# Optimization experiments

Hardware: AMD Instinct MI355X
Metric: run time of the kernel (lower is better)

Reference implementation:

```python
import jax, jax.numpy as jnp
import numpy as np

N_RNA, N_ATAC = 4096, 8192
IN_C, HID, H = 256, 128, 2
DH = HID // H
TOPK, THR = 10, 0.8


def setup_inputs() -> dict:
    key = jax.random.key(0)
    ks = jax.random.split(key, 16)
    s = 0.02
    inp = {
        'x_rna': jax.random.normal(ks[0], (N_RNA, IN_C), jnp.float32),
        'x_atac': jax.random.normal(ks[1], (N_ATAC, IN_C), jnp.float32),
        'chrom_mask': (jax.random.uniform(ks[2], (N_RNA, N_ATAC)) > 0.5).astype(jnp.float32),
        'Wq': jax.random.normal(ks[3], (IN_C, HID)) * s, 'bq': jnp.zeros((HID,)),
        'Wk': jax.random.normal(ks[4], (IN_C, HID)) * s, 'bk': jnp.zeros((HID,)),
        'Wvr': jax.random.normal(ks[5], (IN_C, HID)) * s, 'bvr': jnp.zeros((HID,)),
        'Wva': jax.random.normal(ks[6], (IN_C, HID)) * s, 'bva': jnp.zeros((HID,)),
        'Wor': jax.random.normal(ks[7], (HID, HID)) * s, 'bor': jnp.zeros((HID,)),
        'Woa': jax.random.normal(ks[8], (HID, HID)) * s, 'boa': jnp.zeros((HID,)),
        'Wsr': jax.random.normal(ks[9], (IN_C, HID)) * s, 'bsr': jnp.zeros((HID,)),
        'Wsa': jax.random.normal(ks[10], (IN_C, HID)) * s, 'bsa': jnp.zeros((HID,)),
        'Wdr': jax.random.normal(ks[11], (2 * HID, HID)) * s, 'bdr': jnp.zeros((HID,)),
        'Wda': jax.random.normal(ks[12], (2 * HID, HID)) * s, 'bda': jnp.zeros((HID,)),
    }
    return inp


def reference(x_rna, x_atac, chrom_mask, Wq, bq, Wk, bk, Wvr, bvr, Wva, bva,
              Wor, bor, Woa, boa, Wsr, bsr, Wsa, bsa, Wdr, bdr, Wda, bda):
    # projections -> [N, H, DH]
    q = (x_rna @ Wq + bq).reshape(N_RNA, H, DH)
    k = (x_atac @ Wk + bk).reshape(N_ATAC, H, DH)
    v_a = (x_atac @ Wva + bva).reshape(N_ATAC, H, DH)
    v_r = (x_rna @ Wvr + bvr).reshape(N_RNA, H, DH)

    # raw attention [H, N_rna, N_atac], biological mask, sigmoid
    att = jnp.einsum('rhd,ahd->hra', q, k) * chrom_mask[None]
    att = jax.nn.sigmoid(att)
    thr_mask = (att > THR).astype(att.dtype)

    # top-k sparsify + softmax over selected values, scatter back
    topv, topi = jax.lax.top_k(att, TOPK)          # [H, N_rna, K]
    topv = jax.nn.softmax(topv, axis=-1)
    i_h = jnp.arange(H)[:, None, None]
    i_r = jnp.arange(N_RNA)[None, :, None]
    sparse = jnp.zeros_like(att).at[i_h, i_r, topi].set(topv)
    att = sparse * thr_mask

    # aggregations (second bmm and its transpose)
    rna_agg = jnp.einsum('hra,ahd->rhd', att, v_a).reshape(N_RNA, HID)
    atac_agg = jnp.einsum('hra,rhd->ahd', att, v_r).reshape(N_ATAC, HID)

    # out proj (num_heads > 1), self attention concat, dim reduction
    rna_agg = rna_agg @ Wor + bor
    atac_agg = atac_agg @ Woa + boa
    rna_agg = jnp.concatenate([rna_agg, x_rna @ Wsr + bsr], axis=1)
    atac_agg = jnp.concatenate([atac_agg, x_atac @ Wsa + bsa], axis=1)
    return (rna_agg @ Wdr + bdr, atac_agg @ Wda + bda)
```

## Files before the change

kernel.cpp:

```cpp
#include <hip/hip_runtime.h>
#include <math.h>

#define N_RNA 4096
#define N_ATAC 8192
#define IN_C 256
#define HID 128
#define NH 2
#define TOPK 10
#define CAP 32
#define NCHUNK 8
#define TAU_EPS 0.12f
#define NEG_INF -3.402823466e38f

typedef __attribute__((ext_vector_type(8))) short bf16x8;
typedef __attribute__((ext_vector_type(4))) float f32x4;

static __device__ __forceinline__ f32x4 mfma16(bf16x8 a, bf16x8 b, f32x4 c) {
    return __builtin_amdgcn_mfma_f32_16x16x32_bf16(a, b, c, 0, 0, 0);
}

static __device__ __forceinline__ unsigned short f2bf(float f) {
    unsigned int u = __float_as_uint(f);
    unsigned int r = (u + 0x7fffu + ((u >> 16) & 1u)) >> 16;
    return (unsigned short)r;
}
static __device__ __forceinline__ float bf2f(unsigned short h) {
    return __uint_as_float(((unsigned int)h) << 16);
}

__global__ __launch_bounds__(256) void prep_all(
    const float* __restrict__ mask, unsigned int* __restrict__ bits2,
    float* __restrict__ atac_agg,
    const float* __restrict__ Wor, const float* __restrict__ bor,
    const float* __restrict__ Woa, const float* __restrict__ boa,
    const float* __restrict__ Wsr, const float* __restrict__ bsr,
    const float* __restrict__ Wsa, const float* __restrict__ bsa,
    const float* __restrict__ Wdr, const float* __restrict__ bdr,
    const float* __restrict__ Wda, const float* __restrict__ bda,
    float* __restrict__ Wr1, float* __restrict__ Wr2, float* __restrict__ br,
    float* __restrict__ Wa1, float* __restrict__ Wa2, float* __restrict__ ba,
    const float* __restrict__ x_rna, const float* __restrict__ x_atac,
    const float* __restrict__ Wq, const float* __restrict__ bq,
    const float* __restrict__ Wk, const float* __restrict__ bk,
    const float* __restrict__ Wvr, const float* __restrict__ bvr,
    const float* __restrict__ Wva, const float* __restrict__ bva,
    unsigned short* __restrict__ qhi, unsigned short* __restrict__ qlo,
    unsigned short* __restrict__ khf_hi, unsigned short* __restrict__ khf_lo,
    float* __restrict__ v_r, float* __restrict__ v_a) {
    __shared__ __align__(16) float x_s[32][33];
    __shared__ __align__(16) float w_s[32][128];
    int bx = blockIdx.x;
    int tid = threadIdx.x;

    if (bx >= 768 && bx < 1792) {
        int e = bx - 768;
        int rt = e >> 4, ac = e & 15;
        int a0 = ac * 512 + tid * 2;
        int r0 = rt * 64;
        unsigned int w0[2] = {0, 0}, w1[2] = {0, 0};
#pragma unroll 8
        for (int rr = 0; rr < 32; ++rr) {
            float2 m0 = *(const float2*)&mask[(size_t)(r0 + rr) * N_ATAC + a0];
            float2 m1 = *(const float2*)&mask[(size_t)(r0 + 32 + rr) * N_ATAC + a0];
            w0[0] |= ((m0.x > 0.5f) ? 1u : 0u) << rr;
            w0[1] |= ((m0.y > 0.5f) ? 1u : 0u) << rr;
            w1[0] |= ((m1.x > 0.5f) ? 1u : 0u) << rr;
            w1[1] |= ((m1.y > 0.5f) ? 1u : 0u) << rr;
        }
        uint4 o = make_uint4(w0[0], w1[0], w0[1], w1[1]);
        *(uint4*)&bits2[((size_t)rt * N_ATAC + a0) * 2] = o;
        return;
    }
    if (bx >= 1792 && bx < 2048) {
        size_t i = ((size_t)(bx - 1792) * 256 + tid) * 16;
        float4 z = make_float4(0.f, 0.f, 0.f, 0.f);
        *(float4*)&atac_agg[i] = z;
        *(float4*)&atac_agg[i + 4] = z;
        *(float4*)&atac_agg[i + 8] = z;
        *(float4*)&atac_agg[i + 12] = z;
        return;
    }
    if (bx >= 2048) {
        int f = (bx - 2048) * 256 + tid;
        if (f < 16384) {
            int i = f >> 7, j = f & 127; float s = 0.f;
            for (int t = 0; t < 128; ++t) s += Wor[i * 128 + t] * Wdr[t * 128 + j];
            Wr1[f] = s;
        } else if (f < 49152) {
            int e = f - 16384; int i = e >> 7, j = e & 127; float s = 0.f;
            for (int t = 0; t < 128; ++t) s += Wsr[i * 128 + t] * Wdr[(128 + t) * 128 + j];
            Wr2[e] = s;
        } else if (f < 65536) {
            int e = f - 49152; int i = e >> 7, j = e & 127; float s = 0.f;
            for (int t = 0; t < 128; ++t) s += Woa[i * 128 + t] * Wda[t * 128 + j];
            Wa1[e] = s;
        } else if (f < 98304) {
            int e = f - 65536; int i = e >> 7, j = e & 127; float s = 0.f;
            for (int t = 0; t < 128; ++t) s += Wsa[i * 128 + t] * Wda[(128 + t) * 128 + j];
            Wa2[e] = s;
        } else if (f < 98432) {
            int j = f - 98304; float s = bdr[j];
            for (int t = 0; t < 128; ++t) s += bor[t] * Wdr[t * 128 + j] + bsr[t] * Wdr[(128 + t) * 128 + j];
            br[j] = s;
        } else if (f < 98560) {
            int j = f - 98432; float s = bda[j];
            for (int t = 0; t < 128; ++t) s += boa[t] * Wda[t * 128 + j] + bsa[t] * Wda[(128 + t) * 128 + j];
            ba[j] = s;
        }
        return;
    }

    int e = bx;
    int cfg, rblk;
    if (e < 128)      { cfg = 0; rblk = e; }
    else if (e < 256) { cfg = 1; rblk = e - 128; }
    else if (e < 512) { cfg = 2; rblk = e - 256; }
    else              { cfg = 3; rblk = e - 512; }
    const float *X, *W, *B;
    if (cfg == 0)      { X = x_rna;  W = Wq;  B = bq;  }
    else if (cfg == 1) { X = x_rna;  W = Wvr; B = bvr; }
    else if (cfg == 2) { X = x_atac; W = Wk;  B = bk;  }
    else               { X = x_atac; W = Wva; B = bva; }
    int r0 = rblk * 32;
    int rg = tid >> 4, cg = tid & 15;

    float acc[2][8];
#pragma unroll
    for (int i = 0; i < 2; ++i)
#pragma unroll
        for (int j = 0; j < 8; ++j) acc[i][j] = 0.f;

    for (int k0 = 0; k0 < IN_C; k0 += 32) {
        __syncthreads();
        {
            int rr = tid >> 3, kq = tid & 7;
            float4 v = *(const float4*)&X[(size_t)(r0 + rr) * IN_C + k0 + kq * 4];
            x_s[rr][kq * 4 + 0] = v.x; x_s[rr][kq * 4 + 1] = v.y;
            x_s[rr][kq * 4 + 2] = v.z; x_s[rr][kq * 4 + 3] = v.w;
        }
        for (int i4 = tid; i4 < 1024; i4 += 256) {
            int kk = i4 >> 5, cq = i4 & 31;
            float4 v = *(const float4*)&W[(size_t)(k0 + kk) * HID + cq * 4];
            *(float4*)&w_s[kk][cq * 4] = v;
        }
        __syncthreads();
#pragma unroll 8
        for (int kk = 0; kk < 32; ++kk) {
            float x0 = x_s[rg * 2 + 0][kk], x1 = x_s[rg * 2 + 1][kk];
            float4 wa = *(const float4*)&w_s[kk][cg * 4];
            float4 wb = *(const float4*)&w_s[kk][64 + cg * 4];
            acc[0][0] += x0 * wa.x; acc[0][1] += x0 * wa.y; acc[0][2] += x0 * wa.z; acc[0][3] += x0 * wa.w;
            acc[0][4] += x0 * wb.x; acc[0][5] += x0 * wb.y; acc[0][6] += x0 * wb.z; acc[0][7] += x0 * wb.w;
            acc[1][0] += x1 * wa.x; acc[1][1] += x1 * wa.y; acc[1][2] += x1 * wa.z; acc[1][3] += x1 * wa.w;
            acc[1][4] += x1 * wb.x; acc[1][5] += x1 * wb.y; acc[1][6] += x1 * wb.z; acc[1][7] += x1 * wb.w;
        }
    }
    float bv[8];
#pragma unroll
    for (int j = 0; j < 8; ++j) {
        int c = (j < 4) ? (cg * 4 + j) : (64 + cg * 4 + (j - 4));
        bv[j] = B[c];
    }
    if (cfg == 0 || cfg == 2) {
#pragma unroll
        for (int i = 0; i < 2; ++i) {
            int r = r0 + rg * 2 + i;
            float va[8];
#pragma unroll
            for (int j = 0; j < 8; ++j) va[j] = acc[i][j] + bv[j];
            ushort4 h0, l0, h1, l1;
            h0.x = f2bf(va[0]); h0.y = f2bf(va[1]); h0.z = f2bf(va[2]); h0.w = f2bf(va[3]);
            h1.x = f2bf(va[4]); h1.y = f2bf(va[5]); h1.z = f2bf(va[6]); h1.w = f2bf(va[7]);
            l0.x = f2bf(va[0] - bf2f(h0.x)); l0.y = f2bf(va[1] - bf2f(h0.y));
            l0.z = f2bf(va[2] - bf2f(h0.z)); l0.w = f2bf(va[3] - bf2f(h0.w));
            l1.x = f2bf(va[4] - bf2f(h1.x)); l1.y = f2bf(va[5] - bf2f(h1.y));
            l1.z = f2bf(va[6] - bf2f(h1.z)); l1.w = f2bf(va[7] - bf2f(h1.w));
            if (cfg == 0) {
                size_t o0 = (size_t)r * 64 + cg * 4;
                size_t o1 = (size_t)(N_RNA + r) * 64 + cg * 4;
                *(ushort4*)&qhi[o0] = h0; *(ushort4*)&qhi[o1] = h1;
                *(ushort4*)&qlo[o0] = l0; *(ushort4*)&qlo[o1] = l1;
            } else {
                int at = r >> 4, n = r & 15;
                int kc = cg >> 1, ee = (cg & 1) * 4;
                size_t o0 = ((size_t)(at) * 8 + kc) * 128 + n * 8 + ee;
                size_t o1 = ((size_t)(512 + at) * 8 + kc) * 128 + n * 8 + ee;
                *(ushort4*)&khf_hi[o0] = h0; *(ushort4*)&khf_hi[o1] = h1;
                *(ushort4*)&khf_lo[o0] = l0; *(ushort4*)&khf_lo[o1] = l1;
            }
        }
    } else {
        float* C = (cfg == 1) ? v_r : v_a;
#pragma unroll
        for (int i = 0; i < 2; ++i) {
            int r = r0 + rg * 2 + i;
            float4 oa = make_float4(acc[i][0] + bv[0], acc[i][1] + bv[1], acc[i][2] + bv[2], acc[i][3] + bv[3]);
            float4 ob = make_float4(acc[i][4] + bv[4], acc[i][5] + bv[5], acc[i][6] + bv[6], acc[i][7] + bv[7]);
            *(float4*)&C[(size_t)r * HID + cg * 4] = oa;
            *(float4*)&C[(size_t)r * HID + 64 + cg * 4] = ob;
        }
    }
}

__global__ __launch_bounds__(256, 4) void attn2(
    const unsigned short* __restrict__ qhi, const unsigned short* __restrict__ qlo,
    const unsigned short* __restrict__ khf_hi, const unsigned short* __restrict__ khf_lo,
    const unsigned int* __restrict__ bits2,
    int* __restrict__ scnt, float* __restrict__ sval, int* __restrict__ sidx) {
    int hq = blockIdx.x; int h = hq >> 3, chunk = hq & 7;
    int rt = blockIdx.y; int r0 = rt * 32;
    int tid = threadIdx.x;
    int w = tid >> 6, lane = tid & 63;
    int n = lane & 15, quad = lane >> 4;
    int q4 = quad * 4;
    int at0 = chunk * 64 + w * 16;
    int hbase = h * 512;
    int rt64 = rt >> 1, word = rt & 1;

    __shared__ __align__(16) float smem[32 * 65];
    __shared__ float taus[32];
    __shared__ int   lcnt[32];

    const bf16x8* kh8 = (const bf16x8*)khf_hi;
    const bf16x8* kl8 = (const bf16x8*)khf_lo;

    bf16x8 Ah[2][2], Al[2][2];
#pragma unroll
    for (int mt = 0; mt < 2; ++mt)
#pragma unroll
        for (int c = 0; c < 2; ++c) {
            size_t off = ((size_t)h * N_RNA + r0 + mt * 16 + n) * 64 + c * 32 + quad * 8;
            Ah[mt][c] = *(const bf16x8*)(qhi + off);
            Al[mt][c] = *(const bf16x8*)(qlo + off);
        }

    float mx[2][4];
#pragma unroll
    for (int mt = 0; mt < 2; ++mt)
#pragma unroll
        for (int i = 0; i < 4; ++i) mx[mt][i] = 0.f;

#pragma unroll 2
    for (int t = 0; t < 16; ++t) {
        int at = at0 + t;
        size_t bidx = ((size_t)hbase + at) * 128 + lane;
        bf16x8 Bh0 = kh8[bidx];
        bf16x8 Bh1 = kh8[bidx + 64];
        unsigned int bw = bits2[((size_t)rt64 * N_ATAC + at * 16 + n) * 2 + word];

        f32x4 S[2];
#pragma unroll
        for (int mt = 0; mt < 2; ++mt) {
            f32x4 s = {0.f, 0.f, 0.f, 0.f};
            s = mfma16(Ah[mt][0], Bh0, s);
            s = mfma16(Ah[mt][1], Bh1, s);
            S[mt] = s;
        }
#pragma unroll
        for (int mt = 0; mt < 2; ++mt) {
            unsigned int sh = bw >> ((mt << 4) + q4);
#pragma unroll
            for (int i = 0; i < 4; ++i) {
                float v = ((sh >> i) & 1) ? S[mt][i] : 0.f;
                mx[mt][i] = fmaxf(mx[mt][i], v);
            }
        }
    }

    {
        int b = w * 16 + n;
#pragma unroll
        for (int mt = 0; mt < 2; ++mt)
#pragma unroll
            for (int i = 0; i < 4; ++i) smem[(mt * 16 + q4 + i) * 65 + b] = mx[mt][i];
    }
    __syncthreads();
    {
        int row = tid >> 3, sub = tid & 7;
        float v[8];
#pragma unroll
        for (int j = 0; j < 8; ++j) v[j] = smem[row * 65 + sub * 8 + j];
        float t10 = 0.f;
#pragma unroll
        for (int s = 0; s < 10; ++s) {
            float bv = v[0]; int bj = 0;
#pragma unroll
            for (int j = 1; j < 8; ++j) if (v[j] > bv) { bv = v[j]; bj = j; }
            int meta = (sub << 3) | bj;
#pragma unroll
            for (int off = 1; off < 8; off <<= 1) {
                float ov = __shfl_xor(bv, off);
                int om = __shfl_xor(meta, off);
                if (ov > bv || (ov == bv && om < meta)) { bv = ov; meta = om; }
            }
            if ((meta >> 3) == sub) v[meta & 7] = -1.f;
            t10 = bv;
        }
        if (sub == 0) taus[row] = t10 - TAU_EPS;
        if (tid < 32) lcnt[tid] = 0;
    }
    __syncthreads();

    float tau[2][4];
#pragma unroll
    for (int mt = 0; mt < 2; ++mt)
#pragma unroll
        for (int i = 0; i < 4; ++i) tau[mt][i] = taus[mt * 16 + q4 + i];

    float* lval = smem;
    int*   lidx = (int*)(smem + 1024);

#pragma unroll 2
    for (int t = 0; t < 16; ++t) {
        int at = at0 + t;
        size_t bidx = ((size_t)hbase + at) * 128 + lane;
        bf16x8 Bh0 = kh8[bidx];
        bf16x8 Bh1 = kh8[bidx + 64];
        bf16x8 Bl0 = kl8[bidx];
        bf16x8 Bl1 = kl8[bidx + 64];
        unsigned int bw = bits2[((size_t)rt64 * N_ATAC + at * 16 + n) * 2 + word];

        f32x4 S[2];
#pragma unroll
        for (int mt = 0; mt < 2; ++mt) {
            f32x4 s = {0.f, 0.f, 0.f, 0.f};
            s = mfma16(Ah[mt][0], Bh0, s);
            s = mfma16(Ah[mt][1], Bh1, s);
            s = mfma16(Ah[mt][0], Bl0, s);
            s = mfma16(Ah[mt][1], Bl1, s);
            s = mfma16(Al[mt][0], Bh0, s);
            s = mfma16(Al[mt][1], Bh1, s);
            S[mt] = s;
        }
        int a16 = at * 16 + n;
#pragma unroll
        for (int mt = 0; mt < 2; ++mt) {
            unsigned int sh = bw >> ((mt << 4) + q4);
#pragma unroll
            for (int i = 0; i < 4; ++i) {
                if (((sh >> i) & 1) && S[mt][i] >= tau[mt][i]) {
                    int row = mt * 16 + q4 + i;
                    int pos = atomicAdd(&lcnt[row], 1);
                    if (pos < CAP) { lval[row * CAP + pos] = S[mt][i]; lidx[row * CAP + pos] = a16; }
                }
            }
        }
    }
    __syncthreads();

    if (tid < 32) {
        int c = lcnt[tid]; if (c > CAP) c = CAP;
        scnt[((size_t)h * N_RNA + r0 + tid) * NCHUNK + chunk] = c;
    }
    {
        int row = tid >> 3, j0 = tid & 7;
        int c = lcnt[row]; if (c > CAP) c = CAP;
        size_t slot = ((size_t)h * N_RNA + r0 + row) * NCHUNK + chunk;
        for (int j = j0; j < c; j += 8) {
            sval[slot * CAP + j] = lval[row * CAP + j];
            sidx[slot * CAP + j] = lidx[row * CAP + j];
        }
    }
}

__global__ __launch_bounds__(256) void fin_agg(
    const int* __restrict__ scnt, const float* __restrict__ sval, const int* __restrict__ sidx,
    const float* __restrict__ v_a, const float* __restrict__ v_r,
    float* __restrict__ rna_agg, float* __restrict__ atac_agg) {
    int wid = threadIdx.x >> 6, lane = threadIdx.x & 63;
    int p = blockIdx.x * 4 + wid;
    int h = p >> 12, r = p & 4095;
    size_t sbase = (size_t)p * NCHUNK;

    float val[4]; int aidx[4];
#pragma unroll
    for (int j = 0; j < 4; ++j) {
        int e = j * 64 + lane;
        int chunk = e >> 5, pos = e & 31;
        int c = scnt[sbase + chunk];
        size_t sl = (sbase + chunk) * CAP + pos;
        bool ok = pos < c;
        val[j] = ok ? sval[sl] : NEG_INF;
        aidx[j] = ok ? sidx[sl] : 0;
    }

    float sv[10]; int si[10];
#pragma unroll
    for (int s = 0; s < 10; ++s) {
        float bv = val[0]; int bj = 0;
#pragma unroll
        for (int j = 1; j < 4; ++j) if (val[j] > bv) { bv = val[j]; bj = j; }
        int bmeta = (bj << 6) | lane;
#pragma unroll
        for (int off = 32; off >= 1; off >>= 1) {
            float ov = __shfl_xor(bv, off);
            int om = __shfl_xor(bmeta, off);
            if (ov > bv || (ov == bv && om < bmeta)) { bv = ov; bmeta = om; }
        }
        int wj = bmeta >> 6, wl = bmeta & 63;
        if (lane == wl) {
#pragma unroll
            for (int j = 0; j < 4; ++j) if (j == wj) val[j] = NEG_INF;
        }
        int av = aidx[0];
#pragma unroll
        for (int j = 1; j < 4; ++j) if (wj == j) av = aidx[j];
        sv[s] = bv;
        si[s] = __shfl(av, wl);
    }

    float wgt[10]; float sum = 0.f; float sg[10];
#pragma unroll
    for (int s = 0; s < 10; ++s) {
        sg[s] = 1.0f / (1.0f + expf(-sv[s]));
        float es = expf(sg[s]);
        wgt[s] = es;
        sum += es;
    }
    float inv = 1.0f / sum;
#pragma unroll
    for (int s = 0; s < 10; ++s) {
        wgt[s] *= inv;
        if (!(sg[s] > 0.8f)) wgt[s] = 0.f;
    }

    float acc = 0.f;
#pragma unroll
    for (int s = 0; s < 10; ++s) {
        float vv = v_a[(size_t)si[s] * HID + h * 64 + lane];
        acc += wgt[s] * vv;
    }
    rna_agg[(size_t)r * HID + h * 64 + lane] = acc;

    float vr = v_r[(size_t)r * HID + h * 64 + lane];
#pragma unroll
    for (int s = 0; s < 10; ++s) {
        if (wgt[s] != 0.f) {
            atomicAdd(&atac_agg[(size_t)si[s] * HID + h * 64 + lane], wgt[s] * vr);
        }
    }
}

__global__ __launch_bounds__(256) void out_gemm(
    const float* __restrict__ rna_agg, const float* __restrict__ x_rna,
    const float* __restrict__ Wr1, const float* __restrict__ Wr2, const float* __restrict__ brf,
    const float* __restrict__ atac_agg, const float* __restrict__ x_atac,
    const float* __restrict__ Wa1, const float* __restrict__ Wa2, const float* __restrict__ baf,
    float* __restrict__ out_r, float* __restrict__ out_a) {
    __shared__ __align__(16) float x_s[32][33];
    __shared__ __align__(16) float w_s[32][128];
    int bx = blockIdx.x;
    const float *A, *X, *W1, *W2, *bias; float* C;
    int r0;
    if (bx < 128) { A = rna_agg; X = x_rna; W1 = Wr1; W2 = Wr2; bias = brf; C = out_r; r0 = bx * 32; }
    else { A = atac_agg; X = x_atac; W1 = Wa1; W2 = Wa2; bias = baf; C = out_a; r0 = (bx - 128) * 32; }
    int tid = threadIdx.x;
    int rg = tid >> 4, cg = tid & 15;

    float acc[2][8];
#pragma unroll
    for (int i = 0; i < 2; ++i)
#pragma unroll
        for (int j = 0; j < 8; ++j) acc[i][j] = 0.f;

    for (int k0 = 0; k0 < 384; k0 += 32) {
        __syncthreads();
        {
            int rr = tid >> 3, kq = tid & 7;
            float4 v;
            if (k0 < 128) v = *(const float4*)&A[(size_t)(r0 + rr) * HID + k0 + kq * 4];
            else          v = *(const float4*)&X[(size_t)(r0 + rr) * IN_C + (k0 - 128) + kq * 4];
            x_s[rr][kq * 4 + 0] = v.x; x_s[rr][kq * 4 + 1] = v.y;
            x_s[rr][kq * 4 + 2] = v.z; x_s[rr][kq * 4 + 3] = v.w;
        }
        for (int i4 = tid; i4 < 1024; i4 += 256) {
            int kk = i4 >> 5, cq = i4 & 31;
            float4 v;
            if (k0 < 128) v = *(const float4*)&W1[(size_t)(k0 + kk) * HID + cq * 4];
            else          v = *(const float4*)&W2[(size_t)(k0 - 128 + kk) * HID + cq * 4];
            *(float4*)&w_s[kk][cq * 4] = v;
        }
        __syncthreads();
#pragma unroll 8
        for (int kk = 0; kk < 32; ++kk) {
            float x0 = x_s[rg * 2 + 0][kk], x1 = x_s[rg * 2 + 1][kk];
            float4 wa = *(const float4*)&w_s[kk][cg * 4];
            float4 wb = *(const float4*)&w_s[kk][64 + cg * 4];
            acc[0][0] += x0 * wa.x; acc[0][1] += x0 * wa.y; acc[0][2] += x0 * wa.z; acc[0][3] += x0 * wa.w;
            acc[0][4] += x0 * wb.x; acc[0][5] += x0 * wb.y; acc[0][6] += x0 * wb.z; acc[0][7] += x0 * wb.w;
            acc[1][0] += x1 * wa.x; acc[1][1] += x1 * wa.y; acc[1][2] += x1 * wa.z; acc[1][3] += x1 * wa.w;
            acc[1][4] += x1 * wb.x; acc[1][5] += x1 * wb.y; acc[1][6] += x1 * wb.z; acc[1][7] += x1 * wb.w;
        }
    }
    float bv[8];
#pragma unroll
    for (int j = 0; j < 8; ++j) {
        int c = (j < 4) ? (cg * 4 + j) : (64 + cg * 4 + (j - 4));
        bv[j] = bias[c];
    }
#pragma unroll
    for (int i = 0; i < 2; ++i) {
        int r = r0 + rg * 2 + i;
        float4 oa = make_float4(acc[i][0] + bv[0], acc[i][1] + bv[1], acc[i][2] + bv[2], acc[i][3] + bv[3]);
        float4 ob = make_float4(acc[i][4] + bv[4], acc[i][5] + bv[5], acc[i][6] + bv[6], acc[i][7] + bv[7]);
        *(float4*)&C[(size_t)r * HID + cg * 4] = oa;
        *(float4*)&C[(size_t)r * HID + 64 + cg * 4] = ob;
    }
}

extern "C" void kernel_launch(void* const* d_in, const int* in_sizes, int n_in,
                              void* d_out, int out_size, void* d_ws, size_t ws_size,
                              hipStream_t stream) {
    const float* x_rna = (const float*)d_in[0];
    const float* x_atac = (const float*)d_in[1];
    const float* mask = (const float*)d_in[2];
    const float* Wq = (const float*)d_in[3];  const float* bq = (const float*)d_in[4];
    const float* Wk = (const float*)d_in[5];  const float* bk = (const float*)d_in[6];
    const float* Wvr = (const float*)d_in[7]; const float* bvr = (const float*)d_in[8];
    const float* Wva = (const float*)d_in[9]; const float* bva = (const float*)d_in[10];
    const float* Wor = (const float*)d_in[11]; const float* bor = (const float*)d_in[12];
    const float* Woa = (const float*)d_in[13]; const float* boa = (const float*)d_in[14];
    const float* Wsr = (const float*)d_in[15]; const float* bsr = (const float*)d_in[16];
    const float* Wsa = (const float*)d_in[17]; const float* bsa = (const float*)d_in[18];
    const float* Wdr = (const float*)d_in[19]; const float* bdr = (const float*)d_in[20];
    const float* Wda = (const float*)d_in[21]; const float* bda = (const float*)d_in[22];

    float* out_r = (float*)d_out;
    float* out_a = out_r + N_RNA * HID;

    float* ws = (float*)d_ws;
    unsigned short* qhi = (unsigned short*)ws;
    unsigned short* qlo = qhi + 524288;
    unsigned short* khf_hi = qlo + 524288;
    unsigned short* khf_lo = khf_hi + 1048576;
    unsigned int* bits2 = (unsigned int*)(ws + 1572864);
    float* v_r = ws + 1572864 + 1048576;
    float* v_a = v_r + 524288;
    float* Wr1 = v_a + 1048576;
    float* Wr2 = Wr1 + 16384;
    float* brf = Wr2 + 32768;
    float* Wa1 = brf + 128;
    float* Wa2 = Wa1 + 16384;
    float* baf = Wa2 + 32768;
    int* scnt = (int*)(baf + 128);
    float* sval = (float*)scnt + 65536;
    int* sidx = (int*)(sval + 2097152);
    float* rna_agg = (float*)sidx + 2097152;
    float* atac_agg = rna_agg + 524288;

    hipLaunchKernelGGL(prep_all, dim3(2434), dim3(256), 0, stream,
                       mask, bits2, atac_agg,
                       Wor, bor, Woa, boa, Wsr, bsr, Wsa, bsa, Wdr, bdr, Wda, bda,
                       Wr1, Wr2, brf, Wa1, Wa2, baf,
                       x_rna, x_atac, Wq, bq, Wk, bk, Wvr, bvr, Wva, bva,
                       qhi, qlo, khf_hi, khf_lo, v_r, v_a);
    hipLaunchKernelGGL(attn2, dim3(16, 128), dim3(256), 0, stream,
                       qhi, qlo, khf_hi, khf_lo, bits2, scnt, sval, sidx);
    hipLaunchKernelGGL(fin_agg, dim3(2048), dim3(256), 0, stream,
                       scnt, sval, sidx, v_a, v_r, rna_agg, atac_agg);
    hipLaunchKernelGGL(out_gemm, dim3(384), dim3(256), 0, stream,
                       rna_agg, x_rna, Wr1, Wr2, brf,
                       atac_agg, x_atac, Wa1, Wa2, baf, out_r, out_a);
}
```

Baseline: 420.4 us.

## Move projection and output GEMMs to split-bf16 MFMA with pre-transposed weights

Replaces the FP32 FMA inner loops of the input projections and the fused output GEMM with bf16 MFMA, using a hi/lo split (three MFMAs per tile) to keep near-FP32 accuracy. A new wprep kernel transposes and splits the weights into bf16 hi/lo arrays ahead of time and folds the weight-combining products. The mask bit-packing blocks also now process four columns per thread. This adds an extra kernel launch and scalar scattered epilogue stores in exchange for much cheaper matrix math.

```diff
diff --git a/kernel.cpp b/kernel.cpp
--- a/kernel.cpp
+++ b/kernel.cpp
@@ -28,51 +28,129 @@
     return __uint_as_float(((unsigned int)h) << 16);
 }
 
-__global__ __launch_bounds__(256) void prep_all(
-    const float* __restrict__ mask, unsigned int* __restrict__ bits2,
-    float* __restrict__ atac_agg,
+__global__ __launch_bounds__(256) void wprep(
+    const float* __restrict__ Wq, const float* __restrict__ Wk,
+    const float* __restrict__ Wvr, const float* __restrict__ Wva,
     const float* __restrict__ Wor, const float* __restrict__ bor,
     const float* __restrict__ Woa, const float* __restrict__ boa,
     const float* __restrict__ Wsr, const float* __restrict__ bsr,
     const float* __restrict__ Wsa, const float* __restrict__ bsa,
     const float* __restrict__ Wdr, const float* __restrict__ bdr,
     const float* __restrict__ Wda, const float* __restrict__ bda,
-    float* __restrict__ Wr1, float* __restrict__ Wr2, float* __restrict__ br,
-    float* __restrict__ Wa1, float* __restrict__ Wa2, float* __restrict__ ba,
+    unsigned short* __restrict__ wt, unsigned short* __restrict__ wrf,
+    unsigned short* __restrict__ waf,
+    float* __restrict__ brf, float* __restrict__ baf) {
+    int bx = blockIdx.x, tid = threadIdx.x;
+    if (bx < 32) {
+        int cfg = bx >> 3, k0 = (bx & 7) * 32;
+        const float* W = (cfg == 0) ? Wq : (cfg == 1) ? Wvr : (cfg == 2) ? Wk : Wva;
+        __shared__ float ts[32][132];
+#pragma unroll
+        for (int rep = 0; rep < 4; ++rep) {
+            int id = rep * 256 + tid; int kk = id >> 5, cq = id & 31;
+            float4 v = *(const float4*)&W[(size_t)(k0 + kk) * HID + cq * 4];
+            ts[kk][cq * 4 + 0] = v.x; ts[kk][cq * 4 + 1] = v.y;
+            ts[kk][cq * 4 + 2] = v.z; ts[kk][cq * 4 + 3] = v.w;
+        }
+        __syncthreads();
+        int col = tid >> 1, seg = tid & 1;
+        unsigned short hb[16], lb[16];
+#pragma unroll
+        for (int u = 0; u < 16; ++u) {
+            float f = ts[seg * 16 + u][col];
+            unsigned short h = f2bf(f);
+            hb[u] = h; lb[u] = f2bf(f - bf2f(h));
+        }
+        unsigned short* hp = wt + cfg * 65536;
+        unsigned short* lp = hp + 32768;
+        size_t o = (size_t)col * 256 + k0 + seg * 16;
+#pragma unroll
+        for (int u4 = 0; u4 < 4; ++u4) {
+            ushort4 th, tl;
+            th.x = hb[u4 * 4]; th.y = hb[u4 * 4 + 1]; th.z = hb[u4 * 4 + 2]; th.w = hb[u4 * 4 + 3];
+            tl.x = lb[u4 * 4]; tl.y = lb[u4 * 4 + 1]; tl.z = lb[u4 * 4 + 2]; tl.w = lb[u4 * 4 + 3];
+            *(ushort4*)&hp[o + u4 * 4] = th;
+            *(ushort4*)&lp[o + u4 * 4] = tl;
+        }
+        return;
+    }
+    int f = (bx - 32) * 256 + tid;
+    if (f < 16384) {
+        int i = f >> 7, j = f & 127; float s = 0.f;
+        for (int t = 0; t < 128; ++t) s += Wor[i * 128 + t] * Wdr[t * 128 + j];
+        unsigned short h = f2bf(s);
+        wrf[(size_t)j * 128 + i] = h;
+        wrf[16384 + (size_t)j * 128 + i] = f2bf(s - bf2f(h));
+    } else if (f < 49152) {
+        int e = f - 16384; int i = e >> 7, j = e & 127; float s = 0.f;
+        for (int t = 0; t < 128; ++t) s += Wsr[i * 128 + t] * Wdr[(128 + t) * 128 + j];
+        unsigned short h = f2bf(s);
+        wrf[32768 + (size_t)j * 256 + i] = h;
+        wrf[65536 + (size_t)j * 256 + i] = f2bf(s - bf2f(h));
+    } else if (f < 65536) {
+        int e = f - 49152; int i = e >> 7, j = e & 127; float s = 0.f;
+        for (int t = 0; t < 128; ++t) s += Woa[i * 128 + t] * Wda[t * 128 + j];
+        unsigned short h = f2bf(s);
+        waf[(size_t)j * 128 + i] = h;
+        waf[16384 + (size_t)j * 128 + i] = f2bf(s - bf2f(h));
+    } else if (f < 98304) {
+        int e = f - 65536; int i = e >> 7, j = e & 127; float s = 0.f;
+        for (int t = 0; t < 128; ++t) s += Wsa[i * 128 + t] * Wda[(128 + t) * 128 + j];
+        unsigned short h = f2bf(s);
+        waf[32768 + (size_t)j * 256 + i] = h;
+        waf[65536 + (size_t)j * 256 + i] = f2bf(s - bf2f(h));
+    } else if (f < 98432) {
+        int j = f - 98304; float s = bdr[j];
+        for (int t = 0; t < 128; ++t) s += bor[t] * Wdr[t * 128 + j] + bsr[t] * Wdr[(128 + t) * 128 + j];
+        brf[j] = s;
+    } else if (f < 98560) {
+        int j = f - 98432; float s = bda[j];
+        for (int t = 0; t < 128; ++t) s += boa[t] * Wda[t * 128 + j] + bsa[t] * Wda[(128 + t) * 128 + j];
+        baf[j] = s;
+    }
+}
+
+__global__ __launch_bounds__(256) void prep_all(
+    const float* __restrict__ mask, unsigned int* __restrict__ bits2,
+    float* __restrict__ atac_agg,
     const float* __restrict__ x_rna, const float* __restrict__ x_atac,
-    const float* __restrict__ Wq, const float* __restrict__ bq,
-    const float* __restrict__ Wk, const float* __restrict__ bk,
-    const float* __restrict__ Wvr, const float* __restrict__ bvr,
-    const float* __restrict__ Wva, const float* __restrict__ bva,
+    const unsigned short* __restrict__ wt,
+    const float* __restrict__ bq, const float* __restrict__ bk,
+    const float* __restrict__ bvr, const float* __restrict__ bva,
     unsigned short* __restrict__ qhi, unsigned short* __restrict__ qlo,
     unsigned short* __restrict__ khf_hi, unsigned short* __restrict__ khf_lo,
     float* __restrict__ v_r, float* __restrict__ v_a) {
-    __shared__ __align__(16) float x_s[32][33];
-    __shared__ __align__(16) float w_s[32][128];
-    int bx = blockIdx.x;
-    int tid = threadIdx.x;
-
-    if (bx >= 768 && bx < 1792) {
+    __shared__ __align__(16) unsigned short ah_s[32 * 40];
+    __shared__ __align__(16) unsigned short al_s[32 * 40];
+    int bx = blockIdx.x, tid = threadIdx.x;
+
+    if (bx >= 768 && bx < 1280) {
         int e = bx - 768;
-        int rt = e >> 4, ac = e & 15;
-        int a0 = ac * 512 + tid * 2;
+        int rt = e >> 3, ac = e & 7;
+        int a0 = ac * 1024 + tid * 4;
         int r0 = rt * 64;
-        unsigned int w0[2] = {0, 0}, w1[2] = {0, 0};
+        unsigned int w0[4] = {0, 0, 0, 0}, w1[4] = {0, 0, 0, 0};
 #pragma unroll 8
         for (int rr = 0; rr < 32; ++rr) {
-            float2 m0 = *(const float2*)&mask[(size_t)(r0 + rr) * N_ATAC + a0];
-            float2 m1 = *(const float2*)&mask[(size_t)(r0 + 32 + rr) * N_ATAC + a0];
+            float4 m0 = *(const float4*)&mask[(size_t)(r0 + rr) * N_ATAC + a0];
+            float4 m1 = *(const float4*)&mask[(size_t)(r0 + 32 + rr) * N_ATAC + a0];
             w0[0] |= ((m0.x > 0.5f) ? 1u : 0u) << rr;
             w0[1] |= ((m0.y > 0.5f) ? 1u : 0u) << rr;
+            w0[2] |= ((m0.z > 0.5f) ? 1u : 0u) << rr;
+            w0[3] |= ((m0.w > 0.5f) ? 1u : 0u) << rr;
             w1[0] |= ((m1.x > 0.5f) ? 1u : 0u) << rr;
             w1[1] |= ((m1.y > 0.5f) ? 1u : 0u) << rr;
-        }
-        uint4 o = make_uint4(w0[0], w1[0], w0[1], w1[1]);
-        *(uint4*)&bits2[((size_t)rt * N_ATAC + a0) * 2] = o;
+            w1[2] |= ((m1.z > 0.5f) ? 1u : 0u) << rr;
+            w1[3] |= ((m1.w > 0.5f) ? 1u : 0u) << rr;
+        }
+        uint4 oA = make_uint4(w0[0], w1[0], w0[1], w1[1]);
+        uint4 oB = make_uint4(w0[2], w1[2], w0[3], w1[3]);
+        *(uint4*)&bits2[((size_t)rt * N_ATAC + a0) * 2] = oA;
+        *(uint4*)&bits2[((size_t)rt * N_ATAC + a0) * 2 + 4] = oB;
         return;
     }
-    if (bx >= 1792 && bx < 2048) {
-        size_t i = ((size_t)(bx - 1792) * 256 + tid) * 16;
+    if (bx >= 1280) {
+        size_t i = ((size_t)(bx - 1280) * 256 + tid) * 16;
         float4 z = make_float4(0.f, 0.f, 0.f, 0.f);
         *(float4*)&atac_agg[i] = z;
         *(float4*)&atac_agg[i + 4] = z;
@@ -80,125 +158,104 @@
         *(float4*)&atac_agg[i + 12] = z;
         return;
     }
-    if (bx >= 2048) {
-        int f = (bx - 2048) * 256 + tid;
-        if (f < 16384) {
-            int i = f >> 7, j = f & 127; float s = 0.f;
-            for (int t = 0; t < 128; ++t) s += Wor[i * 128 + t] * Wdr[t * 128 + j];
-            Wr1[f] = s;
-        } else if (f < 49152) {
-            int e = f - 16384; int i = e >> 7, j = e & 127; float s = 0.f;
-            for (int t = 0; t < 128; ++t) s += Wsr[i * 128 + t] * Wdr[(128 + t) * 128 + j];
-            Wr2[e] = s;
-        } else if (f < 65536) {
-            int e = f - 49152; int i = e >> 7, j = e & 127; float s = 0.f;
-            for (int t = 0; t < 128; ++t) s += Woa[i * 128 + t] * Wda[t * 128 + j];
-            Wa1[e] = s;
-        } else if (f < 98304) {
-            int e = f - 65536; int i = e >> 7, j = e & 127; float s = 0.f;
-            for (int t = 0; t < 128; ++t) s += Wsa[i * 128 + t] * Wda[(128 + t) * 128 + j];
-            Wa2[e] = s;
-        } else if (f < 98432) {
-            int j = f - 98304; float s = bdr[j];
-            for (int t = 0; t < 128; ++t) s += bor[t] * Wdr[t * 128 + j] + bsr[t] * Wdr[(128 + t) * 128 + j];
-            br[j] = s;
-        } else if (f < 98560) {
-            int j = f - 98432; float s = bda[j];
-            for (int t = 0; t < 128; ++t) s += boa[t] * Wda[t * 128 + j] + bsa[t] * Wda[(128 + t) * 128 + j];
-            ba[j] = s;
-        }
-        return;
-    }
-
-    int e = bx;
+
     int cfg, rblk;
-    if (e < 128)      { cfg = 0; rblk = e; }
-    else if (e < 256) { cfg = 1; rblk = e - 128; }
-    else if (e < 512) { cfg = 2; rblk = e - 256; }
-    else              { cfg = 3; rblk = e - 512; }
-    const float *X, *W, *B;
-    if (cfg == 0)      { X = x_rna;  W = Wq;  B = bq;  }
-    else if (cfg == 1) { X = x_rna;  W = Wvr; B = bvr; }
-    else if (cfg == 2) { X = x_atac; W = Wk;  B = bk;  }
-    else               { X = x_atac; W = Wva; B = bva; }
+    if (bx < 128)      { cfg = 0; rblk = bx; }
+    else if (bx < 256) { cfg = 1; rblk = bx - 128; }
+    else if (bx < 512) { cfg = 2; rblk = bx - 256; }
+    else               { cfg = 3; rblk = bx - 512; }
+    const float* X = (cfg <= 1) ? x_rna : x_atac;
+    const float* Bv = (cfg == 0) ? bq : (cfg == 1) ? bvr : (cfg == 2) ? bk : bva;
+    const unsigned short* wth = wt + cfg * 65536;
+    const unsigned short* wtl = wth + 32768;
     int r0 = rblk * 32;
-    int rg = tid >> 4, cg = tid & 15;
-
-    float acc[2][8];
-#pragma unroll
-    for (int i = 0; i < 2; ++i)
-#pragma unroll
-        for (int j = 0; j < 8; ++j) acc[i][j] = 0.f;
+    int w = tid >> 6, lane = tid & 63, n = lane & 15, quad = lane >> 4;
+
+    const f32x4 zf = {0.f, 0.f, 0.f, 0.f};
+    f32x4 acc[2][2];
+#pragma unroll
+    for (int mt = 0; mt < 2; ++mt)
+#pragma unroll
+        for (int nt = 0; nt < 2; ++nt) acc[mt][nt] = zf;
 
     for (int k0 = 0; k0 < IN_C; k0 += 32) {
         __syncthreads();
         {
             int rr = tid >> 3, kq = tid & 7;
             float4 v = *(const float4*)&X[(size_t)(r0 + rr) * IN_C + k0 + kq * 4];
-            x_s[rr][kq * 4 + 0] = v.x; x_s[rr][kq * 4 + 1] = v.y;
-            x_s[rr][kq * 4 + 2] = v.z; x_s[rr][kq * 4 + 3] = v.w;
-        }
-        for (int i4 = tid; i4 < 1024; i4 += 256) {
-            int kk = i4 >> 5, cq = i4 & 31;
-            float4 v = *(const float4*)&W[(size_t)(k0 + kk) * HID + cq * 4];
-            *(float4*)&w_s[kk][cq * 4] = v;
+            ushort4 h, l;
+            h.x = f2bf(v.x); h.y = f2bf(v.y); h.z = f2bf(v.z); h.w = f2bf(v.w);
+            l.x = f2bf(v.x - bf2f(h.x)); l.y = f2bf(v.y - bf2f(h.y));
+            l.z = f2bf(v.z - bf2f(h.z)); l.w = f2bf(v.w - bf2f(h.w));
+            *(ushort4*)&ah_s[rr * 40 + kq * 4] = h;
+            *(ushort4*)&al_s[rr * 40 + kq * 4] = l;
         }
         __syncthreads();
-#pragma unroll 8
-        for (int kk = 0; kk < 32; ++kk) {
-            float x0 = x_s[rg * 2 + 0][kk], x1 = x_s[rg * 2 + 1][kk];
-            float4 wa = *(const float4*)&w_s[kk][cg * 4];
-            float4 wb = *(const float4*)&w_s[kk][64 + cg * 4];
-            acc[0][0] += x0 * wa.x; acc[0][1] += x0 * wa.y; acc[0][2] += x0 * wa.z; acc[0][3] += x0 * wa.w;
-            acc[0][4] += x0 * wb.x; acc[0][5] += x0 * wb.y; acc[0][6] += x0 * wb.z; acc[0][7] += x0 * wb.w;
-            acc[1][0] += x1 * wa.x; acc[1][1] += x1 * wa.y; acc[1][2] += x1 * wa.z; acc[1][3] += x1 * wa.w;
-            acc[1][4] += x1 * wb.x; acc[1][5] += x1 * wb.y; acc[1][6] += x1 * wb.z; acc[1][7] += x1 * wb.w;
-        }
-    }
-    float bv[8];
-#pragma unroll
-    for (int j = 0; j < 8; ++j) {
-        int c = (j < 4) ? (cg * 4 + j) : (64 + cg * 4 + (j - 4));
-        bv[j] = B[c];
-    }
-    if (cfg == 0 || cfg == 2) {
-#pragma unroll
-        for (int i = 0; i < 2; ++i) {
-            int r = r0 + rg * 2 + i;
-            float va[8];
-#pragma unroll
-            for (int j = 0; j < 8; ++j) va[j] = acc[i][j] + bv[j];
-            ushort4 h0, l0, h1, l1;
-            h0.x = f2bf(va[0]); h0.y = f2bf(va[1]); h0.z = f2bf(va[2]); h0.w = f2bf(va[3]);
-            h1.x = f2bf(va[4]); h1.y = f2bf(va[5]); h1.z = f2bf(va[6]); h1.w = f2bf(va[7]);
-            l0.x = f2bf(va[0] - bf2f(h0.x)); l0.y = f2bf(va[1] - bf2f(h0.y));
-            l0.z = f2bf(va[2] - bf2f(h0.z)); l0.w = f2bf(va[3] - bf2f(h0.w));
-            l1.x = f2bf(va[4] - bf2f(h1.x)); l1.y = f2bf(va[5] - bf2f(h1.y));
-            l1.z = f2bf(va[6] - bf2f(h1.z)); l1.w = f2bf(va[7] - bf2f(h1.w));
-            if (cfg == 0) {
-                size_t o0 = (size_t)r * 64 + cg * 4;
-                size_t o1 = (size_t)(N_RNA + r) * 64 + cg * 4;
-                *(ushort4*)&qhi[o0] = h0; *(ushort4*)&qhi[o1] = h1;
-                *(ushort4*)&qlo[o0] = l0; *(ushort4*)&qlo[o1] = l1;
-            } else {
-                int at = r >> 4, n = r & 15;
-                int kc = cg >> 1, ee = (cg & 1) * 4;
-                size_t o0 = ((size_t)(at) * 8 + kc) * 128 + n * 8 + ee;
-                size_t o1 = ((size_t)(512 + at) * 8 + kc) * 128 + n * 8 + ee;
-                *(ushort4*)&khf_hi[o0] = h0; *(ushort4*)&khf_hi[o1] = h1;
-                *(ushort4*)&khf_lo[o0] = l0; *(ushort4*)&khf_lo[o1] = l1;
+        bf16x8 Afh[2], Afl[2];
+#pragma unroll
+        for (int mt = 0; mt < 2; ++mt) {
+            Afh[mt] = *(const bf16x8*)&ah_s[(mt * 16 + n) * 40 + quad * 8];
+            Afl[mt] = *(const bf16x8*)&al_s[(mt * 16 + n) * 40 + quad * 8];
+        }
+#pragma unroll
+        for (int nt = 0; nt < 2; ++nt) {
+            int c = w * 32 + nt * 16 + n;
+            size_t o = (size_t)c * 256 + k0 + quad * 8;
+            bf16x8 Bh = *(const bf16x8*)&wth[o];
+            bf16x8 Bl = *(const bf16x8*)&wtl[o];
+#pragma unroll
+            for (int mt = 0; mt < 2; ++mt) {
+                acc[mt][nt] = mfma16(Afh[mt], Bh, acc[mt][nt]);
+                acc[mt][nt] = mfma16(Afh[mt], Bl, acc[mt][nt]);
+                acc[mt][nt] = mfma16(Afl[mt], Bh, acc[mt][nt]);
             }
         }
+    }
+    float bvx[2];
+    bvx[0] = Bv[w * 32 + n]; bvx[1] = Bv[w * 32 + 16 + n];
+    if (cfg == 1 || cfg == 3) {
+        float* C = (cfg == 1) ? v_r : v_a;
+#pragma unroll
+        for (int mt = 0; mt < 2; ++mt)
+#pragma unroll
+            for (int nt = 0; nt < 2; ++nt)
+#pragma unroll
+                for (int i = 0; i < 4; ++i) {
+                    int r = r0 + mt * 16 + quad * 4 + i;
+                    int c = w * 32 + nt * 16 + n;
+                    C[(size_t)r * HID + c] = acc[mt][nt][i] + bvx[nt];
+                }
+    } else if (cfg == 0) {
+#pragma unroll
+        for (int mt = 0; mt < 2; ++mt)
+#pragma unroll
+            for (int nt = 0; nt < 2; ++nt)
+#pragma unroll
+                for (int i = 0; i < 4; ++i) {
+                    int r = r0 + mt * 16 + quad * 4 + i;
+                    int c = w * 32 + nt * 16 + n;
+                    float o = acc[mt][nt][i] + bvx[nt];
+                    int head = c >> 6, ch = c & 63;
+                    size_t off = ((size_t)head * N_RNA + r) * 64 + ch;
+                    unsigned short h = f2bf(o);
+                    qhi[off] = h; qlo[off] = f2bf(o - bf2f(h));
+                }
     } else {
-        float* C = (cfg == 1) ? v_r : v_a;
-#pragma unroll
-        for (int i = 0; i < 2; ++i) {
-            int r = r0 + rg * 2 + i;
-            float4 oa = make_float4(acc[i][0] + bv[0], acc[i][1] + bv[1], acc[i][2] + bv[2], acc[i][3] + bv[3]);
-            float4 ob = make_float4(acc[i][4] + bv[4], acc[i][5] + bv[5], acc[i][6] + bv[6], acc[i][7] + bv[7]);
-            *(float4*)&C[(size_t)r * HID + cg * 4] = oa;
-            *(float4*)&C[(size_t)r * HID + 64 + cg * 4] = ob;
-        }
+#pragma unroll
+        for (int mt = 0; mt < 2; ++mt)
+#pragma unroll
+            for (int nt = 0; nt < 2; ++nt)
+#pragma unroll
+                for (int i = 0; i < 4; ++i) {
+                    int r = r0 + mt * 16 + quad * 4 + i;
+                    int c = w * 32 + nt * 16 + n;
+                    float o = acc[mt][nt][i] + bvx[nt];
+                    int head = c >> 6, ch = c & 63;
+                    size_t off = ((size_t)(head * 512 + (r >> 4)) * 8 + (ch >> 3)) * 128
+                               + (size_t)(r & 15) * 8 + (ch & 7);
+                    unsigned short h = f2bf(o);
+                    khf_hi[off] = h; khf_lo[off] = f2bf(o - bf2f(h));
+                }
     }
 }
 
@@ -443,25 +500,24 @@
 
 __global__ __launch_bounds__(256) void out_gemm(
     const float* __restrict__ rna_agg, const float* __restrict__ x_rna,
-    const float* __restrict__ Wr1, const float* __restrict__ Wr2, const float* __restrict__ brf,
+    const unsigned short* __restrict__ wrt, const float* __restrict__ brf,
     const float* __restrict__ atac_agg, const float* __restrict__ x_atac,
-    const float* __restrict__ Wa1, const float* __restrict__ Wa2, const float* __restrict__ baf,
+    const unsigned short* __restrict__ wat, const float* __restrict__ baf,
     float* __restrict__ out_r, float* __restrict__ out_a) {
-    __shared__ __align__(16) float x_s[32][33];
-    __shared__ __align__(16) float w_s[32][128];
-    int bx = blockIdx.x;
-    const float *A, *X, *W1, *W2, *bias; float* C;
-    int r0;
-    if (bx < 128) { A = rna_agg; X = x_rna; W1 = Wr1; W2 = Wr2; bias = brf; C = out_r; r0 = bx * 32; }
-    else { A = atac_agg; X = x_atac; W1 = Wa1; W2 = Wa2; bias = baf; C = out_a; r0 = (bx - 128) * 32; }
-    int tid = threadIdx.x;
-    int rg = tid >> 4, cg = tid & 15;
-
-    float acc[2][8];
-#pragma unroll
-    for (int i = 0; i < 2; ++i)
-#pragma unroll
-        for (int j = 0; j < 8; ++j) acc[i][j] = 0.f;
+    __shared__ __align__(16) unsigned short ah_s[32 * 40];
+    __shared__ __align__(16) unsigned short al_s[32 * 40];
+    int bx = blockIdx.x, tid = threadIdx.x;
+    const float *A, *X, *bias; const unsigned short* wb; float* C; int r0;
+    if (bx < 128) { A = rna_agg; X = x_rna; wb = wrt; bias = brf; C = out_r; r0 = bx * 32; }
+    else { A = atac_agg; X = x_atac; wb = wat; bias = baf; C = out_a; r0 = (bx - 128) * 32; }
+    int w = tid >> 6, lane = tid & 63, n = lane & 15, quad = lane >> 4;
+
+    const f32x4 zf = {0.f, 0.f, 0.f, 0.f};
+    f32x4 acc[2][2];
+#pragma unroll
+    for (int mt = 0; mt < 2; ++mt)
+#pragma unroll
+        for (int nt = 0; nt < 2; ++nt) acc[mt][nt] = zf;
 
     for (int k0 = 0; k0 < 384; k0 += 32) {
         __syncthreads();
@@ -470,42 +526,49 @@
             float4 v;
             if (k0 < 128) v = *(const float4*)&A[(size_t)(r0 + rr) * HID + k0 + kq * 4];
             else          v = *(const float4*)&X[(size_t)(r0 + rr) * IN_C + (k0 - 128) + kq * 4];
-            x_s[rr][kq * 4 + 0] = v.x; x_s[rr][kq * 4 + 1] = v.y;
-            x_s[rr][kq * 4 + 2] = v.z; x_s[rr][kq * 4 + 3] = v.w;
-        }
-        for (int i4 = tid; i4 < 1024; i4 += 256) {
-            int kk = i4 >> 5, cq = i4 & 31;
-            float4 v;
-            if (k0 < 128) v = *(const float4*)&W1[(size_t)(k0 + kk) * HID + cq * 4];
-            else          v = *(const float4*)&W2[(size_t)(k0 - 128 + kk) * HID + cq * 4];
-            *(float4*)&w_s[kk][cq * 4] = v;
+            ushort4 h, l;
+            h.x = f2bf(v.x); h.y = f2bf(v.y); h.z = f2bf(v.z); h.w = f2bf(v.w);
+            l.x = f2bf(v.x - bf2f(h.x)); l.y = f2bf(v.y - bf2f(h.y));
+            l.z = f2bf(v.z - bf2f(h.z)); l.w = f2bf(v.w - bf2f(h.w));
+            *(ushort4*)&ah_s[rr * 40 + kq * 4] = h;
+            *(ushort4*)&al_s[rr * 40 + kq * 4] = l;
         }
         __syncthreads();
-#pragma unroll 8
-        for (int kk = 0; kk < 32; ++kk) {
-            float x0 = x_s[rg * 2 + 0][kk], x1 = x_s[rg * 2 + 1][kk];
-            float4 wa = *(const float4*)&w_s[kk][cg * 4];
-            float4 wb = *(const float4*)&w_s[kk][64 + cg * 4];
-            acc[0][0] += x0 * wa.x; acc[0][1] += x0 * wa.y; acc[0][2] += x0 * wa.z; acc[0][3] += x0 * wa.w;
-            acc[0][4] += x0 * wb.x; acc[0][5] += x0 * wb.y; acc[0][6] += x0 * wb.z; acc[0][7] += x0 * wb.w;
-            acc[1][0] += x1 * wa.x; acc[1][1] += x1 * wa.y; acc[1][2] += x1 * wa.z; acc[1][3] += x1 * wa.w;
-            acc[1][4] += x1 * wb.x; acc[1][5] += x1 * wb.y; acc[1][6] += x1 * wb.z; acc[1][7] += x1 * wb.w;
-        }
-    }
-    float bv[8];
-#pragma unroll
-    for (int j = 0; j < 8; ++j) {
-        int c = (j < 4) ? (cg * 4 + j) : (64 + cg * 4 + (j - 4));
-        bv[j] = bias[c];
-    }
-#pragma unroll
-    for (int i = 0; i < 2; ++i) {
-        int r = r0 + rg * 2 + i;
-        float4 oa = make_float4(acc[i][0] + bv[0], acc[i][1] + bv[1], acc[i][2] + bv[2], acc[i][3] + bv[3]);
-        float4 ob = make_float4(acc[i][4] + bv[4], acc[i][5] + bv[5], acc[i][6] + bv[6], acc[i][7] + bv[7]);
-        *(float4*)&C[(size_t)r * HID + cg * 4] = oa;
-        *(float4*)&C[(size_t)r * HID + 64 + cg * 4] = ob;
-    }
+        bf16x8 Afh[2], Afl[2];
+#pragma unroll
+        for (int mt = 0; mt < 2; ++mt) {
+            Afh[mt] = *(const bf16x8*)&ah_s[(mt * 16 + n) * 40 + quad * 8];
+            Afl[mt] = *(const bf16x8*)&al_s[(mt * 16 + n) * 40 + quad * 8];
+        }
+#pragma unroll
+        for (int nt = 0; nt < 2; ++nt) {
+            int c = w * 32 + nt * 16 + n;
+            size_t o;
+            const unsigned short *ph, *pl;
+            if (k0 < 128) { o = (size_t)c * 128 + k0 + quad * 8;         ph = wb;         pl = wb + 16384; }
+            else          { o = (size_t)c * 256 + (k0 - 128) + quad * 8; ph = wb + 32768; pl = wb + 65536; }
+            bf16x8 Bh = *(const bf16x8*)&ph[o];
+            bf16x8 Bl = *(const bf16x8*)&pl[o];
+#pragma unroll
+            for (int mt = 0; mt < 2; ++mt) {
+                acc[mt][nt] = mfma16(Afh[mt], Bh, acc[mt][nt]);
+                acc[mt][nt] = mfma16(Afh[mt], Bl, acc[mt][nt]);
+                acc[mt][nt] = mfma16(Afl[mt], Bh, acc[mt][nt]);
+            }
+        }
+    }
+    float bvx[2];
+    bvx[0] = bias[w * 32 + n]; bvx[1] = bias[w * 32 + 16 + n];
+#pragma unroll
+    for (int mt = 0; mt < 2; ++mt)
+#pragma unroll
+        for (int nt = 0; nt < 2; ++nt)
+#pragma unroll
+            for (int i = 0; i < 4; ++i) {
+                int r = r0 + mt * 16 + quad * 4 + i;
+                int c = w * 32 + nt * 16 + n;
+                C[(size_t)r * HID + c] = acc[mt][nt][i] + bvx[nt];
+            }
 }
 
 extern "C" void kernel_launch(void* const* d_in, const int* in_sizes, int n_in,
@@ -547,18 +610,24 @@
     int* sidx = (int*)(sval + 2097152);
     float* rna_agg = (float*)sidx + 2097152;
     float* atac_agg = rna_agg + 524288;
-
-    hipLaunchKernelGGL(prep_all, dim3(2434), dim3(256), 0, stream,
-                       mask, bits2, atac_agg,
+    unsigned short* wt = (unsigned short*)(atac_agg + 1048576);
+
+    unsigned short* wrf = (unsigned short*)Wr1;
+    unsigned short* waf = (unsigned short*)Wa1;
+
+    hipLaunchKernelGGL(wprep, dim3(417), dim3(256), 0, stream,
+                       Wq, Wk, Wvr, Wva,
                        Wor, bor, Woa, boa, Wsr, bsr, Wsa, bsa, Wdr, bdr, Wda, bda,
-                       Wr1, Wr2, brf, Wa1, Wa2, baf,
-                       x_rna, x_atac, Wq, bq, Wk, bk, Wvr, bvr, Wva, bva,
+                       wt, wrf, waf, brf, baf);
+    hipLaunchKernelGGL(prep_all, dim3(1536), dim3(256), 0, stream,
+                       mask, bits2, atac_agg, x_rna, x_atac, wt,
+                       bq, bk, bvr, bva,
                        qhi, qlo, khf_hi, khf_lo, v_r, v_a);
     hipLaunchKernelGGL(attn2, dim3(16, 128), dim3(256), 0, stream,
                        qhi, qlo, khf_hi, khf_lo, bits2, scnt, sval, sidx);
     hipLaunchKernelGGL(fin_agg, dim3(2048), dim3(256), 0, stream,
                        scnt, sval, sidx, v_a, v_r, rna_agg, atac_agg);
     hipLaunchKernelGGL(out_gemm, dim3(384), dim3(256), 0, stream,
-                       rna_agg, x_rna, Wr1, Wr2, brf,
-                       atac_agg, x_atac, Wa1, Wa2, baf, out_r, out_a);
-}
+                       rna_agg, x_rna, wrf, brf,
+                       atac_agg, x_atac, waf, baf, out_r, out_a);
+}
```

Result: faster. 380.8 us (-9.4%).
